# Optimization experiments

Hardware: AMD Instinct MI355X
Metric: run time of the kernel (lower is better)

Reference implementation:

```python
import jax, jax.numpy as jnp
import numpy as np

HID = 128      # hidden_dim
CDIM = 128     # c_dim
NBLK = 5       # n_blocks
RESO = 32      # grid_resolution
G = RESO ** 3  # number of voxels
B, T = 2, 100000


def setup_inputs() -> dict:
    key = jax.random.key(0)
    ks = jax.random.split(key, 8)
    return {
        "points": jax.random.normal(ks[0], (B, T, 3), jnp.float32),
        "index": jax.random.randint(ks[1], (B, 1, T), 0, G, dtype=jnp.int64),
        # fc_pos: Linear(3, 2*HID)
        "fc_pos_w": jax.random.normal(ks[2], (3, 2 * HID), jnp.float32) * 0.1,
        "fc_pos_b": jnp.zeros((2 * HID,), jnp.float32),
        # ResnetBlockFC(2*HID, HID) x NBLK: fc_0 (2H->H), fc_1 (H->H), shortcut (2H->H, no bias)
        "fc0_w": jax.random.normal(ks[3], (NBLK, 2 * HID, HID), jnp.float32) * 0.05,
        "fc0_b": jnp.zeros((NBLK, HID), jnp.float32),
        "fc1_w": jax.random.normal(ks[4], (NBLK, HID, HID), jnp.float32) * 0.05,
        "fc1_b": jnp.zeros((NBLK, HID), jnp.float32),
        "sc_w": jax.random.normal(ks[5], (NBLK, 2 * HID, HID), jnp.float32) * 0.05,
        # fc_c: Linear(HID, CDIM)
        "fc_c_w": jax.random.normal(ks[6], (HID, CDIM), jnp.float32) * 0.05,
        "fc_c_b": jnp.zeros((CDIM,), jnp.float32),
    }


def _resnet_block(x, w0, b0, w1, b1, ws):
    # ResnetBlockFC: net = fc_0(relu(x)); dx = fc_1(relu(net)); out = shortcut(x) + dx
    net = jnp.maximum(x, 0.0) @ w0 + b0
    dx = jnp.maximum(net, 0.0) @ w1 + b1
    return x @ ws + dx


def reference(points, index, fc_pos_w, fc_pos_b, fc0_w, fc0_b, fc1_w, fc1_b, sc_w, fc_c_w, fc_c_b):
    idx = index[:, 0, :]  # [B, T]

    def pool_local(net):
        # scatter_max over voxels, then gather back per point
        seg = jax.vmap(lambda c_b, i_b: jax.ops.segment_max(c_b, i_b, num_segments=G))(net, idx)  # [B,G,H]
        return jnp.take_along_axis(seg, idx[:, :, None], axis=1)  # [B,T,H]; every gathered voxel is non-empty

    net = points @ fc_pos_w + fc_pos_b          # [B,T,2H]
    net = _resnet_block(net, fc0_w[0], fc0_b[0], fc1_w[0], fc1_b[0], sc_w[0])  # [B,T,H]
    for i in range(1, NBLK):
        pooled = pool_local(net)
        net = jnp.concatenate([net, pooled], axis=2)  # [B,T,2H]
        net = _resnet_block(net, fc0_w[i], fc0_b[i], fc1_w[i], fc1_b[i], sc_w[i])

    c = net @ fc_c_w + fc_c_b  # [B,T,CDIM]

    # generate_grid_features: scatter_mean into the 32^3 grid (zeros for empty voxels)
    sums = jax.vmap(lambda c_b, i_b: jax.ops.segment_sum(c_b, i_b, num_segments=G))(c, idx)  # [B,G,CDIM]
    cnts = jax.vmap(lambda i_b: jax.ops.segment_sum(jnp.ones((T,), c.dtype), i_b, num_segments=G))(idx)  # [B,G]
    cnts = cnts[:, :, None]
    mean = jnp.where(cnts > 0, sums / jnp.maximum(cnts, 1.0), 0.0)
    fea_grid = jnp.transpose(mean, (0, 2, 1)).reshape(B, CDIM, RESO, RESO, RESO)
    return fea_grid
```

## Files before the change

### kernel.cpp

```cpp
#include <hip/hip_runtime.h>

#define T_PTS 100000
#define NB 2
#define GCELLS 32768
#define NCELL (NB * GCELLS)
#define HID 128
#define MBLK 128
#define RBPB 782
#define GRID_RB (NB * RBPB)

typedef __attribute__((ext_vector_type(8))) short bf16x8;
typedef __attribute__((ext_vector_type(4))) float f32x4;

#define MFMA16 __builtin_amdgcn_mfma_f32_16x16x32_bf16

__device__ __forceinline__ unsigned short bf16rne(float f) {
  unsigned u = __float_as_uint(f);
  return (unsigned short)((u + 0x7FFFu + ((u >> 16) & 1u)) >> 16);
}

template <int MODE>
__global__ __launch_bounds__(256, 2) void resblock_mfma(
    const float* __restrict__ src, const float* __restrict__ posw,
    const float* __restrict__ posb, const float* __restrict__ cell,
    const int* __restrict__ idx, const unsigned short* __restrict__ w0p,
    const float* __restrict__ b0, const unsigned short* __restrict__ w1p,
    const float* __restrict__ b1, const unsigned short* __restrict__ swp,
    float* __restrict__ net_out) {
  extern __shared__ unsigned short lds[];
  const int tid = threadIdx.x;
  const int lane = tid & 63;
  const int wid = tid >> 6;
  const int wr = wid >> 1, wc = wid & 1;
  const int b = blockIdx.x / RBPB;
  const int t0 = (blockIdx.x % RBPB) * MBLK;
  const int valid = (T_PTS - t0 < MBLK) ? (T_PTS - t0) : MBLK;

  f32x4 accy[4][4], acco[4][4];
#pragma unroll
  for (int i = 0; i < 4; ++i)
#pragma unroll
    for (int j = 0; j < 4; ++j) {
      f32x4 z = {0.f, 0.f, 0.f, 0.f};
      accy[i][j] = z;
      acco[i][j] = z;
    }

  auto stage = [&](int ks) {
    const int slot = ks & 1;
    const int pt = tid >> 1;
    const int kc = (tid & 1) << 4;
    float xv[16];
    if (MODE == 0) {
      float p0 = 0.f, p1 = 0.f, p2 = 0.f;
      if (pt < valid) {
        const float* pp = src + ((long)b * T_PTS + t0 + pt) * 3;
        p0 = pp[0]; p1 = pp[1]; p2 = pp[2];
      }
      const int kb = ks * 32 + kc;
#pragma unroll
      for (int i = 0; i < 16; i += 4) {
        float4 wa = *(const float4*)(posw + kb + i);
        float4 wb = *(const float4*)(posw + 256 + kb + i);
        float4 wcc = *(const float4*)(posw + 512 + kb + i);
        float4 bb = *(const float4*)(posb + kb + i);
        xv[i + 0] = fmaf(p0, wa.x, fmaf(p1, wb.x, fmaf(p2, wcc.x, bb.x)));
        xv[i + 1] = fmaf(p0, wa.y, fmaf(p1, wb.y, fmaf(p2, wcc.y, bb.y)));
        xv[i + 2] = fmaf(p0, wa.z, fmaf(p1, wb.z, fmaf(p2, wcc.z, bb.z)));
        xv[i + 3] = fmaf(p0, wa.w, fmaf(p1, wb.w, fmaf(p2, wcc.w, bb.w)));
      }
    } else {
      if (pt < valid) {
        if (ks < 4) {
          const float* np =
              src + ((long)b * T_PTS + t0 + pt) * HID + ks * 32 + kc;
#pragma unroll
          for (int i = 0; i < 16; i += 4) {
            float4 v = *(const float4*)(np + i);
            xv[i] = v.x; xv[i + 1] = v.y; xv[i + 2] = v.z; xv[i + 3] = v.w;
          }
        } else {
          const int g = idx[(long)b * T_PTS + t0 + pt];
          const float* cp =
              cell + ((long)b * GCELLS + g) * HID + (ks - 4) * 32 + kc;
#pragma unroll
          for (int i = 0; i < 16; i += 4) {
            float4 v = *(const float4*)(cp + i);
            xv[i] = v.x; xv[i + 1] = v.y; xv[i + 2] = v.z; xv[i + 3] = v.w;
          }
        }
      } else {
#pragma unroll
        for (int i = 0; i < 16; ++i) xv[i] = 0.f;
      }
    }
#pragma unroll
    for (int run = 0; run < 2; ++run) {
      bf16x8 vh, vl, vrh, vrl;
#pragma unroll
      for (int i = 0; i < 8; ++i) {
        float x = xv[run * 8 + i];
        unsigned short h = bf16rne(x);
        float hf = __uint_as_float(((unsigned)h) << 16);
        unsigned short lo = bf16rne(x - hf);
        bool pos = x > 0.f;
        vh[i] = (short)h;
        vl[i] = (short)lo;
        vrh[i] = pos ? (short)h : (short)0;
        vrl[i] = pos ? (short)lo : (short)0;
      }
      const int l = ((kc >> 3) + run) * 16 + (pt & 15);
      const int base = slot * 16384 + (pt >> 4) * 512 + l * 8;
      *(bf16x8*)(lds + base) = vh;
      *(bf16x8*)(lds + base + 4096) = vl;
      *(bf16x8*)(lds + base + 8192) = vrh;
      *(bf16x8*)(lds + base + 12288) = vrl;
    }
  };

  stage(0);
  __syncthreads();

#pragma unroll 1
  for (int ks = 0; ks < 8; ++ks) {
    if (ks < 7) stage(ks + 1);
    const int slot = ks & 1;
    bf16x8 b0h[4], b0l[4], bsh[4], bsl[4];
#pragma unroll
    for (int nt = 0; nt < 4; ++nt) {
      const int fi = (ks * 8 + wc * 4 + nt) * 512 + lane * 8;
      b0h[nt] = *(const bf16x8*)(w0p + fi);
      b0l[nt] = *(const bf16x8*)(w0p + 32768 + fi);
      bsh[nt] = *(const bf16x8*)(swp + fi);
      bsl[nt] = *(const bf16x8*)(swp + 32768 + fi);
    }
#pragma unroll
    for (int mt = 0; mt < 4; ++mt) {
      const int ab = slot * 16384 + (wr * 4 + mt) * 512 + lane * 8;
      bf16x8 axh = *(const bf16x8*)(lds + ab);
      bf16x8 axl = *(const bf16x8*)(lds + ab + 4096);
      bf16x8 arh = *(const bf16x8*)(lds + ab + 8192);
      bf16x8 arl = *(const bf16x8*)(lds + ab + 12288);
#pragma unroll
      for (int nt = 0; nt < 4; ++nt) {
        accy[mt][nt] = MFMA16(arh, b0h[nt], accy[mt][nt], 0, 0, 0);
        accy[mt][nt] = MFMA16(arh, b0l[nt], accy[mt][nt], 0, 0, 0);
        accy[mt][nt] = MFMA16(arl, b0h[nt], accy[mt][nt], 0, 0, 0);
        acco[mt][nt] = MFMA16(axh, bsh[nt], acco[mt][nt], 0, 0, 0);
        acco[mt][nt] = MFMA16(axh, bsl[nt], acco[mt][nt], 0, 0, 0);
        acco[mt][nt] = MFMA16(axl, bsh[nt], acco[mt][nt], 0, 0, 0);
      }
    }
    __syncthreads();
  }

  {
    float b0v[4];
#pragma unroll
    for (int nt = 0; nt < 4; ++nt) b0v[nt] = b0[wc * 64 + nt * 16 + (lane & 15)];
#pragma unroll
    for (int mt = 0; mt < 4; ++mt) {
      const int mt2 = wr * 4 + mt;
#pragma unroll
      for (int nt = 0; nt < 4; ++nt) {
        const int colk = wc * 64 + nt * 16 + (lane & 15);
        const int k2 = colk >> 5;
        const int lg = (colk >> 3) & 3;
        const int j = colk & 7;
#pragma unroll
        for (int r = 0; r < 4; ++r) {
          float h = fmaxf(accy[mt][nt][r] + b0v[nt], 0.f);
          unsigned short hh = bf16rne(h);
          float hf = __uint_as_float(((unsigned)hh) << 16);
          unsigned short hl = bf16rne(h - hf);
          const int l2 = lg * 16 + (lane >> 4) * 4 + r;
          const int o = k2 * 4096 + mt2 * 512 + l2 * 8 + j;
          lds[o] = hh;
          lds[o + 16384] = hl;
        }
      }
    }
  }
  __syncthreads();

#pragma unroll
  for (int k2 = 0; k2 < 4; ++k2) {
    bf16x8 bh[4], bl[4];
#pragma unroll
    for (int nt = 0; nt < 4; ++nt) {
      const int fi = (k2 * 8 + wc * 4 + nt) * 512 + lane * 8;
      bh[nt] = *(const bf16x8*)(w1p + fi);
      bl[nt] = *(const bf16x8*)(w1p + 16384 + fi);
    }
#pragma unroll
    for (int mt = 0; mt < 4; ++mt) {
      const int ab = k2 * 4096 + (wr * 4 + mt) * 512 + lane * 8;
      bf16x8 ah = *(const bf16x8*)(lds + ab);
      bf16x8 al = *(const bf16x8*)(lds + ab + 16384);
#pragma unroll
      for (int nt = 0; nt < 4; ++nt) {
        acco[mt][nt] = MFMA16(ah, bh[nt], acco[mt][nt], 0, 0, 0);
        acco[mt][nt] = MFMA16(ah, bl[nt], acco[mt][nt], 0, 0, 0);
        acco[mt][nt] = MFMA16(al, bh[nt], acco[mt][nt], 0, 0, 0);
      }
    }
  }

  {
    float b1v[4];
#pragma unroll
    for (int nt = 0; nt < 4; ++nt) b1v[nt] = b1[wc * 64 + nt * 16 + (lane & 15)];
#pragma unroll
    for (int mt = 0; mt < 4; ++mt) {
#pragma unroll
      for (int r = 0; r < 4; ++r) {
        const int row = wr * 64 + mt * 16 + (lane >> 4) * 4 + r;
        if (row < valid) {
          float* op = net_out + ((long)b * T_PTS + t0 + row) * HID;
#pragma unroll
          for (int nt = 0; nt < 4; ++nt)
            op[wc * 64 + nt * 16 + (lane & 15)] = acco[mt][nt][r] + b1v[nt];
        }
      }
    }
  }
}

__global__ __launch_bounds__(256, 2) void final_mfma(
    float* __restrict__ net, const unsigned short* __restrict__ wcp,
    const float* __restrict__ bc) {
  extern __shared__ unsigned short lds[];
  const int tid = threadIdx.x;
  const int lane = tid & 63;
  const int wid = tid >> 6;
  const int wr = wid >> 1, wc = wid & 1;
  const int b = blockIdx.x / RBPB;
  const int t0 = (blockIdx.x % RBPB) * MBLK;
  const int valid = (T_PTS - t0 < MBLK) ? (T_PTS - t0) : MBLK;

  f32x4 acc[4][4];
#pragma unroll
  for (int i = 0; i < 4; ++i)
#pragma unroll
    for (int j = 0; j < 4; ++j) {
      f32x4 z = {0.f, 0.f, 0.f, 0.f};
      acc[i][j] = z;
    }

  auto stage = [&](int ks) {
    const int slot = ks & 1;
    const int pt = tid >> 1;
    const int kc = (tid & 1) << 4;
    float xv[16];
    if (pt < valid) {
      const float* np = net + ((long)b * T_PTS + t0 + pt) * HID + ks * 32 + kc;
#pragma unroll
      for (int i = 0; i < 16; i += 4) {
        float4 v = *(const float4*)(np + i);
        xv[i] = v.x; xv[i + 1] = v.y; xv[i + 2] = v.z; xv[i + 3] = v.w;
      }
    } else {
#pragma unroll
      for (int i = 0; i < 16; ++i) xv[i] = 0.f;
    }
#pragma unroll
    for (int run = 0; run < 2; ++run) {
      bf16x8 vh, vl;
#pragma unroll
      for (int i = 0; i < 8; ++i) {
        float x = xv[run * 8 + i];
        unsigned short h = bf16rne(x);
        float hf = __uint_as_float(((unsigned)h) << 16);
        unsigned short lo = bf16rne(x - hf);
        vh[i] = (short)h;
        vl[i] = (short)lo;
      }
      const int l = ((kc >> 3) + run) * 16 + (pt & 15);
      const int base = slot * 8192 + (pt >> 4) * 512 + l * 8;
      *(bf16x8*)(lds + base) = vh;
      *(bf16x8*)(lds + base + 4096) = vl;
    }
  };

  stage(0);
  __syncthreads();
#pragma unroll 1
  for (int ks = 0; ks < 4; ++ks) {
    if (ks < 3) stage(ks + 1);
    const int slot = ks & 1;
    bf16x8 bh[4], bl[4];
#pragma unroll
    for (int nt = 0; nt < 4; ++nt) {
      const int fi = (ks * 8 + wc * 4 + nt) * 512 + lane * 8;
      bh[nt] = *(const bf16x8*)(wcp + fi);
      bl[nt] = *(const bf16x8*)(wcp + 16384 + fi);
    }
#pragma unroll
    for (int mt = 0; mt < 4; ++mt) {
      const int ab = slot * 8192 + (wr * 4 + mt) * 512 + lane * 8;
      bf16x8 ah = *(const bf16x8*)(lds + ab);
      bf16x8 al = *(const bf16x8*)(lds + ab + 4096);
#pragma unroll
      for (int nt = 0; nt < 4; ++nt) {
        acc[mt][nt] = MFMA16(ah, bh[nt], acc[mt][nt], 0, 0, 0);
        acc[mt][nt] = MFMA16(ah, bl[nt], acc[mt][nt], 0, 0, 0);
        acc[mt][nt] = MFMA16(al, bh[nt], acc[mt][nt], 0, 0, 0);
      }
    }
    __syncthreads();
  }

  float bcv[4];
#pragma unroll
  for (int nt = 0; nt < 4; ++nt) bcv[nt] = bc[wc * 64 + nt * 16 + (lane & 15)];
#pragma unroll
  for (int mt = 0; mt < 4; ++mt) {
#pragma unroll
    for (int r = 0; r < 4; ++r) {
      const int row = wr * 64 + mt * 16 + (lane >> 4) * 4 + r;
      if (row < valid) {
        float* op = net + ((long)b * T_PTS + t0 + row) * HID;
#pragma unroll
        for (int nt = 0; nt < 4; ++nt)
          op[wc * 64 + nt * 16 + (lane & 15)] = acc[mt][nt][r] + bcv[nt];
      }
    }
  }
}

__global__ void pack_weights(const float* __restrict__ fc0,
                             const float* __restrict__ fc1,
                             const float* __restrict__ sc,
                             const float* __restrict__ fcc,
                             unsigned short* __restrict__ w0p,
                             unsigned short* __restrict__ w1p,
                             unsigned short* __restrict__ swp,
                             unsigned short* __restrict__ wcp) {
  int gid = blockIdx.x * 256 + threadIdx.x;
  const float* src;
  unsigned short* dst;
  int K, e;
  if (gid < 163840) { src = fc0; dst = w0p; K = 256; e = gid; }
  else if (gid < 327680) { src = sc; dst = swp; K = 256; e = gid - 163840; }
  else if (gid < 409600) { src = fc1; dst = w1p; K = 128; e = gid - 327680; }
  else if (gid < 425984) { src = fcc; dst = wcp; K = 128; e = gid - 409600; }
  else return;
  const int mat = e / (K * 128);
  const int r = e - mat * K * 128;
  const int k = r >> 7, n = r & 127;
  const float x = src[e];
  const unsigned short hi = bf16rne(x);
  const float hf = __uint_as_float(((unsigned)hi) << 16);
  const unsigned short lo = bf16rne(x - hf);
  const int ks = k >> 5, lg = (k >> 3) & 3, j = k & 7;
  const int l = lg * 16 + (n & 15), nt = n >> 4;
  unsigned short* mb = dst + (long)mat * K * 256;
  const int off = ((ks * 8 + nt) * 64 + l) * 8 + j;
  mb[off] = hi;
  mb[off + K * 128] = lo;
}

__global__ void zero_i32(int* __restrict__ p, int n) {
  const int i = blockIdx.x * 256 + threadIdx.x;
  if (i < n) p[i] = 0;
}

__global__ void count_csr(const int* __restrict__ idx, int* __restrict__ curs) {
  const int gid = blockIdx.x * 256 + threadIdx.x;
  if (gid >= NB * T_PTS) return;
  const int b = gid / T_PTS;
  atomicAdd(&curs[b * GCELLS + idx[gid]], 1);
}

__global__ __launch_bounds__(1024) void scan_csr(const int* __restrict__ cnt,
                                                 int* __restrict__ offsets) {
  __shared__ int part[1024];
  const int t = threadIdx.x;
  const int base = t * (NCELL / 1024);
  int s = 0;
  for (int i = 0; i < NCELL / 1024; ++i) s += cnt[base + i];
  part[t] = s;
  __syncthreads();
  for (int d = 1; d < 1024; d <<= 1) {
    int v = (t >= d) ? part[t - d] : 0;
    __syncthreads();
    part[t] += v;
    __syncthreads();
  }
  int run = (t == 0) ? 0 : part[t - 1];
  for (int i = 0; i < NCELL / 1024; ++i) {
    offsets[base + i] = run;
    run += cnt[base + i];
  }
  if (t == 1023) offsets[NCELL] = run;
}

__global__ void scatter_csr(const int* __restrict__ idx,
                            const int* __restrict__ offsets,
                            int* __restrict__ curs, int* __restrict__ perm) {
  const int gid = blockIdx.x * 256 + threadIdx.x;
  if (gid >= NB * T_PTS) return;
  const int b = gid / T_PTS;
  const int cellk = b * GCELLS + idx[gid];
  const int slot = offsets[cellk] + atomicAdd(&curs[cellk], 1);
  perm[slot] = gid;
}

__global__ __launch_bounds__(256) void pool_csr(const float* __restrict__ net,
                                                const int* __restrict__ perm,
                                                const int* __restrict__ offsets,
                                                float* __restrict__ cellf) {
  const int cellk = blockIdx.x * 4 + (threadIdx.x >> 6);
  const int lane = threadIdx.x & 63;
  const int s0 = offsets[cellk], s1 = offsets[cellk + 1];
  if (s0 >= s1) return;
  float2 m = {-3.402823466e38f, -3.402823466e38f};
  for (int j = s0; j < s1; ++j) {
    const long row = perm[j];
    float2 v = *(const float2*)(net + row * HID + lane * 2);
    m.x = fmaxf(m.x, v.x);
    m.y = fmaxf(m.y, v.y);
  }
  *(float2*)(cellf + (long)cellk * HID + lane * 2) = m;
}

__global__ __launch_bounds__(256) void cellsum_csr(
    const float* __restrict__ c, const int* __restrict__ perm,
    const int* __restrict__ offsets, float* __restrict__ sums) {
  const int cellk = blockIdx.x * 4 + (threadIdx.x >> 6);
  const int lane = threadIdx.x & 63;
  const int s0 = offsets[cellk], s1 = offsets[cellk + 1];
  if (s0 >= s1) return;
  float2 m = {0.f, 0.f};
  for (int j = s0; j < s1; ++j) {
    const long row = perm[j];
    float2 v = *(const float2*)(c + row * HID + lane * 2);
    m.x += v.x;
    m.y += v.y;
  }
  *(float2*)(sums + (long)cellk * HID + lane * 2) = m;
}

__global__ void mean_kernel(const float* __restrict__ sums,
                            const int* __restrict__ offsets,
                            float* __restrict__ out) {
  const long gid = (long)blockIdx.x * 256 + threadIdx.x;
  if (gid >= (long)NB * HID * GCELLS) return;
  const int g = (int)(gid % GCELLS);
  const int c = (int)((gid / GCELLS) % HID);
  const int b = (int)(gid / ((long)HID * GCELLS));
  const int cellk = b * GCELLS + g;
  const int cnt = offsets[cellk + 1] - offsets[cellk];
  out[gid] = cnt > 0 ? sums[(long)cellk * HID + c] / (float)cnt : 0.f;
}

extern "C" void kernel_launch(void* const* d_in, const int* in_sizes, int n_in,
                              void* d_out, int out_size, void* d_ws,
                              size_t ws_size, hipStream_t stream) {
  const float* points = (const float*)d_in[0];
  const int* idx = (const int*)d_in[1];
  const float* fc_pos_w = (const float*)d_in[2];
  const float* fc_pos_b = (const float*)d_in[3];
  const float* fc0_w = (const float*)d_in[4];
  const float* fc0_b = (const float*)d_in[5];
  const float* fc1_w = (const float*)d_in[6];
  const float* fc1_b = (const float*)d_in[7];
  const float* sc_w = (const float*)d_in[8];
  const float* fc_c_w = (const float*)d_in[9];
  const float* fc_c_b = (const float*)d_in[10];
  float* out = (float*)d_out;

  const long NET_BYTES = (long)NB * T_PTS * HID * 4;
  const long CELL_BYTES = (long)NB * GCELLS * HID * 4;
  float* net = (float*)d_ws;
  float* cellf = (float*)((char*)d_ws + NET_BYTES);
  float* sums = cellf;
  int* offsets = (int*)((char*)d_ws + NET_BYTES + CELL_BYTES);

  unsigned short* packs = (unsigned short*)d_out;
  unsigned short* w0p = packs;
  unsigned short* swp = packs + 327680;
  unsigned short* w1p = packs + 655360;
  unsigned short* wcp = packs + 819200;
  int* curs = (int*)((char*)d_out + (2l << 20));
  int* perm = (int*)((char*)d_out + (3l << 20));

  const int GRID_PTS = (NB * T_PTS + 255) / 256;
  const int GRID_ZERO = (NCELL + 255) / 256;
  const int GRID_CELL = NCELL / 4;
  const int GRID_MEAN = NB * HID * GCELLS / 256;

  pack_weights<<<1664, 256, 0, stream>>>(fc0_w, fc1_w, sc_w, fc_c_w, w0p, w1p,
                                         swp, wcp);

  zero_i32<<<GRID_ZERO, 256, 0, stream>>>(curs, NCELL);
  count_csr<<<GRID_PTS, 256, 0, stream>>>(idx, curs);
  scan_csr<<<1, 1024, 0, stream>>>(curs, offsets);
  zero_i32<<<GRID_ZERO, 256, 0, stream>>>(curs, NCELL);
  scatter_csr<<<GRID_PTS, 256, 0, stream>>>(idx, offsets, curs, perm);

  resblock_mfma<0><<<GRID_RB, 256, 65536, stream>>>(
      points, fc_pos_w, fc_pos_b, nullptr, nullptr, w0p, fc0_b, w1p, fc1_b,
      swp, net);

  for (int i = 1; i < 5; ++i) {
    pool_csr<<<GRID_CELL, 256, 0, stream>>>(net, perm, offsets, cellf);
    resblock_mfma<1><<<GRID_RB, 256, 65536, stream>>>(
        net, nullptr, nullptr, cellf, idx, w0p + (long)i * 65536,
        fc0_b + i * HID, w1p + (long)i * 32768, fc1_b + i * HID,
        swp + (long)i * 65536, net);
  }

  final_mfma<<<GRID_RB, 256, 32768, stream>>>(net, wcp, fc_c_b);
  cellsum_csr<<<GRID_CELL, 256, 0, stream>>>(net, perm, offsets, sums);
  mean_kernel<<<GRID_MEAN, 256, 0, stream>>>(sums, offsets, out);
}
```

Baseline: 865.3 us.

## Halve row tile to 64 points, remap waves to column slices, swizzle LDS

```diff
diff --git a/kernel.cpp b/kernel.cpp
--- a/kernel.cpp
+++ b/kernel.cpp
@@ -5,8 +5,8 @@
 #define GCELLS 32768
 #define NCELL (NB * GCELLS)
 #define HID 128
-#define MBLK 128
-#define RBPB 782
+#define MBLK 64
+#define RBPB 1563
 #define GRID_RB (NB * RBPB)
 
 typedef __attribute__((ext_vector_type(8))) short bf16x8;
@@ -20,27 +20,26 @@
 }
 
 template <int MODE>
-__global__ __launch_bounds__(256, 2) void resblock_mfma(
+__global__ __launch_bounds__(256, 4) void resblock_mfma(
     const float* __restrict__ src, const float* __restrict__ posw,
     const float* __restrict__ posb, const float* __restrict__ cell,
     const int* __restrict__ idx, const unsigned short* __restrict__ w0p,
     const float* __restrict__ b0, const unsigned short* __restrict__ w1p,
     const float* __restrict__ b1, const unsigned short* __restrict__ swp,
     float* __restrict__ net_out) {
-  extern __shared__ unsigned short lds[];
+  __shared__ unsigned short lds[16384];
   const int tid = threadIdx.x;
   const int lane = tid & 63;
-  const int wid = tid >> 6;
-  const int wr = wid >> 1, wc = wid & 1;
+  const int wc = tid >> 6;
   const int b = blockIdx.x / RBPB;
   const int t0 = (blockIdx.x % RBPB) * MBLK;
   const int valid = (T_PTS - t0 < MBLK) ? (T_PTS - t0) : MBLK;
 
-  f32x4 accy[4][4], acco[4][4];
+  f32x4 accy[4][2], acco[4][2];
 #pragma unroll
   for (int i = 0; i < 4; ++i)
 #pragma unroll
-    for (int j = 0; j < 4; ++j) {
+    for (int j = 0; j < 2; ++j) {
       f32x4 z = {0.f, 0.f, 0.f, 0.f};
       accy[i][j] = z;
       acco[i][j] = z;
@@ -48,9 +47,9 @@
 
   auto stage = [&](int ks) {
     const int slot = ks & 1;
-    const int pt = tid >> 1;
-    const int kc = (tid & 1) << 4;
-    float xv[16];
+    const int pt = tid >> 2;
+    const int kc = (tid & 3) << 3;
+    float xv[8];
     if (MODE == 0) {
       float p0 = 0.f, p1 = 0.f, p2 = 0.f;
       if (pt < valid) {
@@ -59,7 +58,7 @@
       }
       const int kb = ks * 32 + kc;
 #pragma unroll
-      for (int i = 0; i < 16; i += 4) {
+      for (int i = 0; i < 8; i += 4) {
         float4 wa = *(const float4*)(posw + kb + i);
         float4 wb = *(const float4*)(posw + 256 + kb + i);
         float4 wcc = *(const float4*)(posw + 512 + kb + i);
@@ -71,51 +70,41 @@
       }
     } else {
       if (pt < valid) {
+        const float* rp;
         if (ks < 4) {
-          const float* np =
-              src + ((long)b * T_PTS + t0 + pt) * HID + ks * 32 + kc;
-#pragma unroll
-          for (int i = 0; i < 16; i += 4) {
-            float4 v = *(const float4*)(np + i);
-            xv[i] = v.x; xv[i + 1] = v.y; xv[i + 2] = v.z; xv[i + 3] = v.w;
-          }
+          rp = src + ((long)b * T_PTS + t0 + pt) * HID + ks * 32 + kc;
         } else {
           const int g = idx[(long)b * T_PTS + t0 + pt];
-          const float* cp =
-              cell + ((long)b * GCELLS + g) * HID + (ks - 4) * 32 + kc;
-#pragma unroll
-          for (int i = 0; i < 16; i += 4) {
-            float4 v = *(const float4*)(cp + i);
-            xv[i] = v.x; xv[i + 1] = v.y; xv[i + 2] = v.z; xv[i + 3] = v.w;
-          }
+          rp = cell + ((long)b * GCELLS + g) * HID + (ks - 4) * 32 + kc;
         }
+        float4 v0 = *(const float4*)(rp);
+        float4 v1 = *(const float4*)(rp + 4);
+        xv[0] = v0.x; xv[1] = v0.y; xv[2] = v0.z; xv[3] = v0.w;
+        xv[4] = v1.x; xv[5] = v1.y; xv[6] = v1.z; xv[7] = v1.w;
       } else {
 #pragma unroll
-        for (int i = 0; i < 16; ++i) xv[i] = 0.f;
-      }
-    }
-#pragma unroll
-    for (int run = 0; run < 2; ++run) {
-      bf16x8 vh, vl, vrh, vrl;
-#pragma unroll
-      for (int i = 0; i < 8; ++i) {
-        float x = xv[run * 8 + i];
-        unsigned short h = bf16rne(x);
-        float hf = __uint_as_float(((unsigned)h) << 16);
-        unsigned short lo = bf16rne(x - hf);
-        bool pos = x > 0.f;
-        vh[i] = (short)h;
-        vl[i] = (short)lo;
-        vrh[i] = pos ? (short)h : (short)0;
-        vrl[i] = pos ? (short)lo : (short)0;
-      }
-      const int l = ((kc >> 3) + run) * 16 + (pt & 15);
-      const int base = slot * 16384 + (pt >> 4) * 512 + l * 8;
-      *(bf16x8*)(lds + base) = vh;
-      *(bf16x8*)(lds + base + 4096) = vl;
-      *(bf16x8*)(lds + base + 8192) = vrh;
-      *(bf16x8*)(lds + base + 12288) = vrl;
-    }
+        for (int i = 0; i < 8; ++i) xv[i] = 0.f;
+      }
+    }
+    bf16x8 vh, vl, vrh, vrl;
+#pragma unroll
+    for (int i = 0; i < 8; ++i) {
+      float x = xv[i];
+      unsigned short h = bf16rne(x);
+      float hf = __uint_as_float(((unsigned)h) << 16);
+      unsigned short lo = bf16rne(x - hf);
+      bool pos = x > 0.f;
+      vh[i] = (short)h;
+      vl[i] = (short)lo;
+      vrh[i] = pos ? (short)h : (short)0;
+      vrl[i] = pos ? (short)lo : (short)0;
+    }
+    const int l = (kc >> 3) * 16 + (pt & 15);
+    const int base = slot * 8192 + (pt >> 4) * 512 + l * 8;
+    *(bf16x8*)(lds + base) = vh;
+    *(bf16x8*)(lds + base + 2048) = vl;
+    *(bf16x8*)(lds + base + 4096) = vrh;
+    *(bf16x8*)(lds + base + 6144) = vrl;
   };
 
   stage(0);
@@ -125,161 +114,176 @@
   for (int ks = 0; ks < 8; ++ks) {
     if (ks < 7) stage(ks + 1);
     const int slot = ks & 1;
-    bf16x8 b0h[4], b0l[4], bsh[4], bsl[4];
-#pragma unroll
-    for (int nt = 0; nt < 4; ++nt) {
-      const int fi = (ks * 8 + wc * 4 + nt) * 512 + lane * 8;
-      b0h[nt] = *(const bf16x8*)(w0p + fi);
-      b0l[nt] = *(const bf16x8*)(w0p + 32768 + fi);
-      bsh[nt] = *(const bf16x8*)(swp + fi);
-      bsl[nt] = *(const bf16x8*)(swp + 32768 + fi);
-    }
+    {
+      bf16x8 bh[2], bl[2];
+#pragma unroll
+      for (int nt = 0; nt < 2; ++nt) {
+        const int fi = (ks * 8 + wc * 2 + nt) * 512 + lane * 8;
+        bh[nt] = *(const bf16x8*)(w0p + fi);
+        bl[nt] = *(const bf16x8*)(w0p + 32768 + fi);
+      }
+#pragma unroll
+      for (int mt = 0; mt < 4; ++mt) {
+        const int ab = slot * 8192 + mt * 512 + lane * 8;
+        bf16x8 arh = *(const bf16x8*)(lds + ab + 4096);
+        bf16x8 arl = *(const bf16x8*)(lds + ab + 6144);
+#pragma unroll
+        for (int nt = 0; nt < 2; ++nt) {
+          accy[mt][nt] = MFMA16(arh, bh[nt], accy[mt][nt], 0, 0, 0);
+          accy[mt][nt] = MFMA16(arh, bl[nt], accy[mt][nt], 0, 0, 0);
+          accy[mt][nt] = MFMA16(arl, bh[nt], accy[mt][nt], 0, 0, 0);
+        }
+      }
+    }
+    {
+      bf16x8 bh[2], bl[2];
+#pragma unroll
+      for (int nt = 0; nt < 2; ++nt) {
+        const int fi = (ks * 8 + wc * 2 + nt) * 512 + lane * 8;
+        bh[nt] = *(const bf16x8*)(swp + fi);
+        bl[nt] = *(const bf16x8*)(swp + 32768 + fi);
+      }
+#pragma unroll
+      for (int mt = 0; mt < 4; ++mt) {
+        const int ab = slot * 8192 + mt * 512 + lane * 8;
+        bf16x8 axh = *(const bf16x8*)(lds + ab);
+        bf16x8 axl = *(const bf16x8*)(lds + ab + 2048);
+#pragma unroll
+        for (int nt = 0; nt < 2; ++nt) {
+          acco[mt][nt] = MFMA16(axh, bh[nt], acco[mt][nt], 0, 0, 0);
+          acco[mt][nt] = MFMA16(axh, bl[nt], acco[mt][nt], 0, 0, 0);
+          acco[mt][nt] = MFMA16(axl, bh[nt], acco[mt][nt], 0, 0, 0);
+        }
+      }
+    }
+    __syncthreads();
+  }
+
+  {
+    float b0v[2];
+#pragma unroll
+    for (int nt = 0; nt < 2; ++nt)
+      b0v[nt] = b0[wc * 32 + nt * 16 + (lane & 15)];
 #pragma unroll
     for (int mt = 0; mt < 4; ++mt) {
-      const int ab = slot * 16384 + (wr * 4 + mt) * 512 + lane * 8;
-      bf16x8 axh = *(const bf16x8*)(lds + ab);
-      bf16x8 axl = *(const bf16x8*)(lds + ab + 4096);
-      bf16x8 arh = *(const bf16x8*)(lds + ab + 8192);
-      bf16x8 arl = *(const bf16x8*)(lds + ab + 12288);
-#pragma unroll
-      for (int nt = 0; nt < 4; ++nt) {
-        accy[mt][nt] = MFMA16(arh, b0h[nt], accy[mt][nt], 0, 0, 0);
-        accy[mt][nt] = MFMA16(arh, b0l[nt], accy[mt][nt], 0, 0, 0);
-        accy[mt][nt] = MFMA16(arl, b0h[nt], accy[mt][nt], 0, 0, 0);
-        acco[mt][nt] = MFMA16(axh, bsh[nt], acco[mt][nt], 0, 0, 0);
-        acco[mt][nt] = MFMA16(axh, bsl[nt], acco[mt][nt], 0, 0, 0);
-        acco[mt][nt] = MFMA16(axl, bsh[nt], acco[mt][nt], 0, 0, 0);
-      }
-    }
-    __syncthreads();
-  }
-
-  {
-    float b0v[4];
-#pragma unroll
-    for (int nt = 0; nt < 4; ++nt) b0v[nt] = b0[wc * 64 + nt * 16 + (lane & 15)];
-#pragma unroll
-    for (int mt = 0; mt < 4; ++mt) {
-      const int mt2 = wr * 4 + mt;
-#pragma unroll
-      for (int nt = 0; nt < 4; ++nt) {
-        const int colk = wc * 64 + nt * 16 + (lane & 15);
-        const int k2 = colk >> 5;
-        const int lg = (colk >> 3) & 3;
-        const int j = colk & 7;
+#pragma unroll
+      for (int nt = 0; nt < 2; ++nt) {
+        const int c = wc * 32 + nt * 16 + (lane & 15);
+        const int k2 = c >> 5;
+        const int j = c & 7;
+        const int lahi = ((c & 31) >> 3) * 16;
 #pragma unroll
         for (int r = 0; r < 4; ++r) {
           float h = fmaxf(accy[mt][nt][r] + b0v[nt], 0.f);
           unsigned short hh = bf16rne(h);
           float hf = __uint_as_float(((unsigned)hh) << 16);
           unsigned short hl = bf16rne(h - hf);
-          const int l2 = lg * 16 + (lane >> 4) * 4 + r;
-          const int o = k2 * 4096 + mt2 * 512 + l2 * 8 + j;
-          lds[o] = hh;
-          lds[o + 16384] = hl;
+          int la = lahi + (lane >> 4) * 4 + r;
+          la ^= (la >> 3) & 7;
+          const int off = ((k2 * 4 + mt) * 64 + la) * 8 + j;
+          lds[off] = hh;
+          lds[off + 8192] = hl;
         }
       }
     }
   }
   __syncthreads();
 
-#pragma unroll
-  for (int k2 = 0; k2 < 4; ++k2) {
-    bf16x8 bh[4], bl[4];
-#pragma unroll
-    for (int nt = 0; nt < 4; ++nt) {
-      const int fi = (k2 * 8 + wc * 4 + nt) * 512 + lane * 8;
-      bh[nt] = *(const bf16x8*)(w1p + fi);
-      bl[nt] = *(const bf16x8*)(w1p + 16384 + fi);
-    }
+  {
+    const int lar = lane ^ ((lane >> 3) & 7);
+#pragma unroll
+    for (int k2 = 0; k2 < 4; ++k2) {
+      bf16x8 bh[2], bl[2];
+#pragma unroll
+      for (int nt = 0; nt < 2; ++nt) {
+        const int fi = (k2 * 8 + wc * 2 + nt) * 512 + lane * 8;
+        bh[nt] = *(const bf16x8*)(w1p + fi);
+        bl[nt] = *(const bf16x8*)(w1p + 16384 + fi);
+      }
+#pragma unroll
+      for (int mt = 0; mt < 4; ++mt) {
+        const int ab = ((k2 * 4 + mt) * 64 + lar) * 8;
+        bf16x8 ah = *(const bf16x8*)(lds + ab);
+        bf16x8 al = *(const bf16x8*)(lds + ab + 8192);
+#pragma unroll
+        for (int nt = 0; nt < 2; ++nt) {
+          acco[mt][nt] = MFMA16(ah, bh[nt], acco[mt][nt], 0, 0, 0);
+          acco[mt][nt] = MFMA16(ah, bl[nt], acco[mt][nt], 0, 0, 0);
+          acco[mt][nt] = MFMA16(al, bh[nt], acco[mt][nt], 0, 0, 0);
+        }
+      }
+    }
+  }
+
+  {
+    float b1v[2];
+#pragma unroll
+    for (int nt = 0; nt < 2; ++nt)
+      b1v[nt] = b1[wc * 32 + nt * 16 + (lane & 15)];
 #pragma unroll
     for (int mt = 0; mt < 4; ++mt) {
-      const int ab = k2 * 4096 + (wr * 4 + mt) * 512 + lane * 8;
-      bf16x8 ah = *(const bf16x8*)(lds + ab);
-      bf16x8 al = *(const bf16x8*)(lds + ab + 16384);
-#pragma unroll
-      for (int nt = 0; nt < 4; ++nt) {
-        acco[mt][nt] = MFMA16(ah, bh[nt], acco[mt][nt], 0, 0, 0);
-        acco[mt][nt] = MFMA16(ah, bl[nt], acco[mt][nt], 0, 0, 0);
-        acco[mt][nt] = MFMA16(al, bh[nt], acco[mt][nt], 0, 0, 0);
-      }
-    }
-  }
-
-  {
-    float b1v[4];
-#pragma unroll
-    for (int nt = 0; nt < 4; ++nt) b1v[nt] = b1[wc * 64 + nt * 16 + (lane & 15)];
-#pragma unroll
-    for (int mt = 0; mt < 4; ++mt) {
 #pragma unroll
       for (int r = 0; r < 4; ++r) {
-        const int row = wr * 64 + mt * 16 + (lane >> 4) * 4 + r;
+        const int row = mt * 16 + (lane >> 4) * 4 + r;
         if (row < valid) {
           float* op = net_out + ((long)b * T_PTS + t0 + row) * HID;
-#pragma unroll
-          for (int nt = 0; nt < 4; ++nt)
-            op[wc * 64 + nt * 16 + (lane & 15)] = acco[mt][nt][r] + b1v[nt];
+          op[wc * 32 + (lane & 15)] = acco[mt][0][r] + b1v[0];
+          op[wc * 32 + 16 + (lane & 15)] = acco[mt][1][r] + b1v[1];
         }
       }
     }
   }
 }
 
-__global__ __launch_bounds__(256, 2) void final_mfma(
+__global__ __launch_bounds__(256, 4) void final_mfma(
     float* __restrict__ net, const unsigned short* __restrict__ wcp,
     const float* __restrict__ bc) {
-  extern __shared__ unsigned short lds[];
+  __shared__ unsigned short lds[8192];
   const int tid = threadIdx.x;
   const int lane = tid & 63;
-  const int wid = tid >> 6;
-  const int wr = wid >> 1, wc = wid & 1;
+  const int wc = tid >> 6;
   const int b = blockIdx.x / RBPB;
   const int t0 = (blockIdx.x % RBPB) * MBLK;
   const int valid = (T_PTS - t0 < MBLK) ? (T_PTS - t0) : MBLK;
 
-  f32x4 acc[4][4];
+  f32x4 acc[4][2];
 #pragma unroll
   for (int i = 0; i < 4; ++i)
 #pragma unroll
-    for (int j = 0; j < 4; ++j) {
+    for (int j = 0; j < 2; ++j) {
       f32x4 z = {0.f, 0.f, 0.f, 0.f};
       acc[i][j] = z;
     }
 
   auto stage = [&](int ks) {
     const int slot = ks & 1;
-    const int pt = tid >> 1;
-    const int kc = (tid & 1) << 4;
-    float xv[16];
+    const int pt = tid >> 2;
+    const int kc = (tid & 3) << 3;
+    float xv[8];
     if (pt < valid) {
-      const float* np = net + ((long)b * T_PTS + t0 + pt) * HID + ks * 32 + kc;
-#pragma unroll
-      for (int i = 0; i < 16; i += 4) {
-        float4 v = *(const float4*)(np + i);
-        xv[i] = v.x; xv[i + 1] = v.y; xv[i + 2] = v.z; xv[i + 3] = v.w;
-      }
+      const float* rp = net + ((long)b * T_PTS + t0 + pt) * HID + ks * 32 + kc;
+      float4 v0 = *(const float4*)(rp);
+      float4 v1 = *(const float4*)(rp + 4);
+      xv[0] = v0.x; xv[1] = v0.y; xv[2] = v0.z; xv[3] = v0.w;
+      xv[4] = v1.x; xv[5] = v1.y; xv[6] = v1.z; xv[7] = v1.w;
     } else {
 #pragma unroll
-      for (int i = 0; i < 16; ++i) xv[i] = 0.f;
-    }
-#pragma unroll
-    for (int run = 0; run < 2; ++run) {
-      bf16x8 vh, vl;
-#pragma unroll
-      for (int i = 0; i < 8; ++i) {
-        float x = xv[run * 8 + i];
-        unsigned short h = bf16rne(x);
-        float hf = __uint_as_float(((unsigned)h) << 16);
-        unsigned short lo = bf16rne(x - hf);
-        vh[i] = (short)h;
-        vl[i] = (short)lo;
-      }
-      const int l = ((kc >> 3) + run) * 16 + (pt & 15);
-      const int base = slot * 8192 + (pt >> 4) * 512 + l * 8;
-      *(bf16x8*)(lds + base) = vh;
-      *(bf16x8*)(lds + base + 4096) = vl;
-    }
+      for (int i = 0; i < 8; ++i) xv[i] = 0.f;
+    }
+    bf16x8 vh, vl;
+#pragma unroll
+    for (int i = 0; i < 8; ++i) {
+      float x = xv[i];
+      unsigned short h = bf16rne(x);
+      float hf = __uint_as_float(((unsigned)h) << 16);
+      unsigned short lo = bf16rne(x - hf);
+      vh[i] = (short)h;
+      vl[i] = (short)lo;
+    }
+    const int l = (kc >> 3) * 16 + (pt & 15);
+    const int base = slot * 4096 + (pt >> 4) * 512 + l * 8;
+    *(bf16x8*)(lds + base) = vh;
+    *(bf16x8*)(lds + base + 2048) = vl;
   };
 
   stage(0);
@@ -288,20 +292,20 @@
   for (int ks = 0; ks < 4; ++ks) {
     if (ks < 3) stage(ks + 1);
     const int slot = ks & 1;
-    bf16x8 bh[4], bl[4];
-#pragma unroll
-    for (int nt = 0; nt < 4; ++nt) {
-      const int fi = (ks * 8 + wc * 4 + nt) * 512 + lane * 8;
+    bf16x8 bh[2], bl[2];
+#pragma unroll
+    for (int nt = 0; nt < 2; ++nt) {
+      const int fi = (ks * 8 + wc * 2 + nt) * 512 + lane * 8;
       bh[nt] = *(const bf16x8*)(wcp + fi);
       bl[nt] = *(const bf16x8*)(wcp + 16384 + fi);
     }
 #pragma unroll
     for (int mt = 0; mt < 4; ++mt) {
-      const int ab = slot * 8192 + (wr * 4 + mt) * 512 + lane * 8;
+      const int ab = slot * 4096 + mt * 512 + lane * 8;
       bf16x8 ah = *(const bf16x8*)(lds + ab);
-      bf16x8 al = *(const bf16x8*)(lds + ab + 4096);
-#pragma unroll
-      for (int nt = 0; nt < 4; ++nt) {
+      bf16x8 al = *(const bf16x8*)(lds + ab + 2048);
+#pragma unroll
+      for (int nt = 0; nt < 2; ++nt) {
         acc[mt][nt] = MFMA16(ah, bh[nt], acc[mt][nt], 0, 0, 0);
         acc[mt][nt] = MFMA16(ah, bl[nt], acc[mt][nt], 0, 0, 0);
         acc[mt][nt] = MFMA16(al, bh[nt], acc[mt][nt], 0, 0, 0);
@@ -310,19 +314,19 @@
     __syncthreads();
   }
 
-  float bcv[4];
-#pragma unroll
-  for (int nt = 0; nt < 4; ++nt) bcv[nt] = bc[wc * 64 + nt * 16 + (lane & 15)];
+  float bcv[2];
+#pragma unroll
+  for (int nt = 0; nt < 2; ++nt)
+    bcv[nt] = bc[wc * 32 + nt * 16 + (lane & 15)];
 #pragma unroll
   for (int mt = 0; mt < 4; ++mt) {
 #pragma unroll
     for (int r = 0; r < 4; ++r) {
-      const int row = wr * 64 + mt * 16 + (lane >> 4) * 4 + r;
+      const int row = mt * 16 + (lane >> 4) * 4 + r;
       if (row < valid) {
         float* op = net + ((long)b * T_PTS + t0 + row) * HID;
-#pragma unroll
-        for (int nt = 0; nt < 4; ++nt)
-          op[wc * 64 + nt * 16 + (lane & 15)] = acc[mt][nt][r] + bcv[nt];
+        op[wc * 32 + (lane & 15)] = acc[mt][0][r] + bcv[0];
+        op[wc * 32 + 16 + (lane & 15)] = acc[mt][1][r] + bcv[1];
       }
     }
   }
@@ -499,19 +503,19 @@
   zero_i32<<<GRID_ZERO, 256, 0, stream>>>(curs, NCELL);
   scatter_csr<<<GRID_PTS, 256, 0, stream>>>(idx, offsets, curs, perm);
 
-  resblock_mfma<0><<<GRID_RB, 256, 65536, stream>>>(
+  resblock_mfma<0><<<GRID_RB, 256, 0, stream>>>(
       points, fc_pos_w, fc_pos_b, nullptr, nullptr, w0p, fc0_b, w1p, fc1_b,
       swp, net);
 
   for (int i = 1; i < 5; ++i) {
     pool_csr<<<GRID_CELL, 256, 0, stream>>>(net, perm, offsets, cellf);
-    resblock_mfma<1><<<GRID_RB, 256, 65536, stream>>>(
+    resblock_mfma<1><<<GRID_RB, 256, 0, stream>>>(
         net, nullptr, nullptr, cellf, idx, w0p + (long)i * 65536,
         fc0_b + i * HID, w1p + (long)i * 32768, fc1_b + i * HID,
         swp + (long)i * 65536, net);
   }
 
-  final_mfma<<<GRID_RB, 256, 32768, stream>>>(net, wcp, fc_c_b);
+  final_mfma<<<GRID_RB, 256, 0, stream>>>(net, wcp, fc_c_b);
   cellsum_csr<<<GRID_CELL, 256, 0, stream>>>(net, perm, offsets, sums);
   mean_kernel<<<GRID_MEAN, 256, 0, stream>>>(sums, offsets, out);
 }
```

After: 784.1 us. 1.1x faster.
